# Performance work log

Hardware: AMD Instinct MI355X
Metric: run time of the kernel (lower is better)

Reference implementation:

```python
import jax, jax.numpy as jnp
import numpy as np

N_NODES = 100000
N_EDGES = 1600000
F_IN = 128
N_GRAPHS = 1000
NUM_CLASSES = 2


def setup_inputs() -> dict:
    key = jax.random.key(0)
    ks = jax.random.split(key, 12)
    x = jax.random.normal(ks[0], (N_NODES, F_IN), jnp.float32)
    edge_index = jax.random.randint(ks[1], (2, N_EDGES), 0, N_NODES, dtype=jnp.int32)
    edge_weight = jnp.ones((N_EDGES,), jnp.float32)
    node_graph_index = jnp.sort(
        jax.random.randint(ks[2], (N_NODES,), 0, N_GRAPHS, dtype=jnp.int32))
    s = 0.05
    params = {
        'W0': jax.random.normal(ks[3], (F_IN, 64), jnp.float32) * s,
        'b0': jnp.zeros((64,), jnp.float32),
        'W1': jax.random.normal(ks[4], (64, 32), jnp.float32) * s,
        'b1': jnp.zeros((32,), jnp.float32),
        'Wm1': jax.random.normal(ks[5], (32, 128), jnp.float32) * s,
        'bm1': jnp.zeros((128,), jnp.float32),
        'Wm2': jax.random.normal(ks[6], (128, NUM_CLASSES), jnp.float32) * s,
        'bm2': jnp.zeros((NUM_CLASSES,), jnp.float32),
    }
    return dict(x=x, edge_index=edge_index, edge_weight=edge_weight,
                node_graph_index=node_graph_index, **params)


def _gcn_norm(edge_index, edge_weight, n_nodes):
    # renormalization trick: add self-loops, D^-1/2 (A+I) D^-1/2
    loop = jnp.arange(n_nodes, dtype=edge_index.dtype)
    src = jnp.concatenate([edge_index[0], loop])
    dst = jnp.concatenate([edge_index[1], loop])
    w = jnp.concatenate([edge_weight, jnp.ones((n_nodes,), edge_weight.dtype)])
    deg = jax.ops.segment_sum(w, dst, num_segments=n_nodes)
    dinv = jnp.where(deg > 0, jax.lax.rsqrt(jnp.maximum(deg, 1e-12)), 0.0)
    norm_w = dinv[src] * w * dinv[dst]
    return src, dst, norm_w


def _gcn_layer(h, src, dst, norm_w, W, b, n_nodes):
    m = h @ W                                # [N, out] dense transform first
    msg = m[src] * norm_w[:, None]           # [E+N, out] irregular gather
    agg = jax.ops.segment_sum(msg, dst, num_segments=n_nodes)
    return jax.nn.relu(agg + b)


def reference(x, edge_index, edge_weight, node_graph_index,
              W0, b0, W1, b1, Wm1, bm1, Wm2, bm2):
    n_nodes = x.shape[0]
    src, dst, norm_w = _gcn_norm(edge_index, edge_weight, n_nodes)
    h = _gcn_layer(x, src, dst, norm_w, W0, b0, n_nodes)   # GCN 64 + relu
    # dropout is identity at inference (training=False default)
    h = _gcn_layer(h, src, dst, norm_w, W1, b1, n_nodes)   # GCN 32 + relu
    g = jax.ops.segment_sum(h, node_graph_index, num_segments=N_GRAPHS)  # sum_pool
    g = jax.nn.relu(g @ Wm1 + bm1)
    logits = g @ Wm2 + bm2
    return logits
```

## Files before the change

kernel.cpp:

```cpp
#include <hip/hip_runtime.h>
#include <hip/hip_bf16.h>

#define F_IN 128
#define NPB 256
#define NPB_SH 8
#define MAXB 512
#define CHUNK 4096
#define CAP 5120

typedef __attribute__((ext_vector_type(8))) short short8;
typedef __attribute__((ext_vector_type(4))) float f32x4;


__device__ __forceinline__ float bf2f(unsigned short u) {
    return __uint_as_float(((unsigned int)u) << 16);
}
__device__ __forceinline__ unsigned short f2bf(float f) {
    unsigned int x = __float_as_uint(f);
    x += 0x7FFFu + ((x >> 16) & 1u);
    return (unsigned short)(x >> 16);
}
__device__ __forceinline__ void bf8_fma(float w, uint4 r, float* a) {
    a[0] = fmaf(w, __uint_as_float(r.x << 16), a[0]);
    a[1] = fmaf(w, __uint_as_float(r.x & 0xFFFF0000u), a[1]);
    a[2] = fmaf(w, __uint_as_float(r.y << 16), a[2]);
    a[3] = fmaf(w, __uint_as_float(r.y & 0xFFFF0000u), a[3]);
    a[4] = fmaf(w, __uint_as_float(r.z << 16), a[4]);
    a[5] = fmaf(w, __uint_as_float(r.z & 0xFFFF0000u), a[5]);
    a[6] = fmaf(w, __uint_as_float(r.w << 16), a[6]);
    a[7] = fmaf(w, __uint_as_float(r.w & 0xFFFF0000u), a[7]);
}

__global__ __launch_bounds__(256) void prep_w_kernel(
    const float* __restrict__ W0, const float* __restrict__ W1,
    unsigned short* __restrict__ W0t, unsigned short* __restrict__ W1t,
    int* __restrict__ gcursor, float* __restrict__ Gbuf,
    int nbucket, int gtot) {
    int t = blockIdx.x * 256 + threadIdx.x;
    int stride = gridDim.x * 256;
    for (int o = t; o < 64 * 128; o += stride) {
        int n = o >> 7, k = o & 127;
        W0t[o] = f2bf(W0[k * 64 + n]);
    }
    for (int o = t; o < 32 * 64; o += stride) {
        int n = o >> 6, k = o & 63;
        W1t[o] = f2bf(W1[k * 32 + n]);
    }
    for (int o = t; o < nbucket; o += stride) gcursor[o] = 0;
    for (int o = t; o < gtot; o += stride) Gbuf[o] = 0.f;
}

__global__ __launch_bounds__(1024) void bucket_fused_kernel(
    const int* __restrict__ src, const int* __restrict__ dst,
    const float* __restrict__ ew, int* __restrict__ gcursor,
    int2* __restrict__ tmp, int E, int nbucket) {
    __shared__ int hist[MAXB];
    __shared__ int gbase[MAXB];
    const int tid = threadIdx.x;
    const int e0 = blockIdx.x * CHUNK;
    const int e1 = min(e0 + CHUNK, E);
    for (int b = tid; b < nbucket; b += 1024) hist[b] = 0;
    __syncthreads();
    const int e = e0 + (tid << 2);
    const bool vec = (e + 4 <= e1);
    const int nsc = vec ? 0 : max(0, e1 - e);
    int4 d4 = make_int4(0, 0, 0, 0);
    if (vec) {
        d4 = *(const int4*)(dst + e);
        atomicAdd(&hist[d4.x >> NPB_SH], 1);
        atomicAdd(&hist[d4.y >> NPB_SH], 1);
        atomicAdd(&hist[d4.z >> NPB_SH], 1);
        atomicAdd(&hist[d4.w >> NPB_SH], 1);
    } else {
        for (int j = 0; j < nsc; ++j) {
            int d = dst[e + j];
            ((int*)&d4)[j] = d;
            atomicAdd(&hist[d >> NPB_SH], 1);
        }
    }
    __syncthreads();
    for (int b = tid; b < nbucket; b += 1024) {
        int h = hist[b];
        gbase[b] = (h > 0) ? atomicAdd(&gcursor[b], h) : 0;
        hist[b] = 0;
    }
    __syncthreads();
    if (vec) {
        int4 s4 = *(const int4*)(src + e);
        float4 w4 = *(const float4*)(ew + e);
        {
            int d = d4.x, b = d >> NPB_SH;
            int r = atomicAdd(&hist[b], 1);
            tmp[(size_t)b * CAP + gbase[b] + r] =
                make_int2(s4.x | ((d & (NPB - 1)) << 17), __float_as_int(w4.x));
        }
        {
            int d = d4.y, b = d >> NPB_SH;
            int r = atomicAdd(&hist[b], 1);
            tmp[(size_t)b * CAP + gbase[b] + r] =
                make_int2(s4.y | ((d & (NPB - 1)) << 17), __float_as_int(w4.y));
        }
        {
            int d = d4.z, b = d >> NPB_SH;
            int r = atomicAdd(&hist[b], 1);
            tmp[(size_t)b * CAP + gbase[b] + r] =
                make_int2(s4.z | ((d & (NPB - 1)) << 17), __float_as_int(w4.z));
        }
        {
            int d = d4.w, b = d >> NPB_SH;
            int r = atomicAdd(&hist[b], 1);
            tmp[(size_t)b * CAP + gbase[b] + r] =
                make_int2(s4.w | ((d & (NPB - 1)) << 17), __float_as_int(w4.w));
        }
    } else {
        for (int j = 0; j < nsc; ++j) {
            int d = ((int*)&d4)[j];
            int b = d >> NPB_SH;
            int r = atomicAdd(&hist[b], 1);
            tmp[(size_t)b * CAP + gbase[b] + r] =
                make_int2(src[e + j] | ((d & (NPB - 1)) << 17), __float_as_int(ew[e + j]));
        }
    }
}

__global__ __launch_bounds__(1024) void csr_kernel(
    const int2* __restrict__ tmp, const int* __restrict__ gcursor,
    int2* __restrict__ es, int* __restrict__ rstart, int* __restrict__ rend,
    float* __restrict__ dinv, int N) {
    __shared__ int cnt[256];
    __shared__ float dw[256];
    __shared__ int off[256];
    __shared__ int cur[256];
    const int t = threadIdx.x;
    const int n0 = blockIdx.x << NPB_SH;
    const size_t seg = (size_t)blockIdx.x * CAP;
    if (t < 256) {
        cnt[t] = 0;
        dw[t] = 0.f;
    }
    __syncthreads();
    const int count = gcursor[blockIdx.x];
    const int pairs = count >> 1;
    for (int i = t; i < pairs; i += 1024) {
        int4 v = *(const int4*)(tmp + seg + 2 * i);
        int d0 = v.x >> 17, d1 = v.z >> 17;
        atomicAdd(&cnt[d0], 1);
        atomicAdd(&dw[d0], __int_as_float(v.y));
        atomicAdd(&cnt[d1], 1);
        atomicAdd(&dw[d1], __int_as_float(v.w));
    }
    if ((count & 1) && t == 0) {
        int2 e2 = tmp[seg + count - 1];
        int d = e2.x >> 17;
        atomicAdd(&cnt[d], 1);
        atomicAdd(&dw[d], __int_as_float(e2.y));
    }
    __syncthreads();
    if (t < 256) off[t] = cnt[t];
    __syncthreads();
    for (int o = 1; o < 256; o <<= 1) {
        int x = 0;
        if (t >= o && t < 256) x = off[t - o];
        __syncthreads();
        if (t < 256) off[t] += x;
        __syncthreads();
    }
    if (t < 256) {
        int v = cnt[t];
        int excl = off[t] - v;
        cur[t] = excl;
        int n = n0 + t;
        if (n < N) {
            rstart[n] = (int)seg + excl;
            rend[n] = (int)seg + excl + v;
            dinv[n] = rsqrtf(fmaxf(1.f + dw[t], 1e-12f));
        }
    }
    __syncthreads();
    for (int i = t; i < pairs; i += 1024) {
        int4 v = *(const int4*)(tmp + seg + 2 * i);
        int d0 = v.x >> 17, d1 = v.z >> 17;
        int r0 = atomicAdd(&cur[d0], 1);
        es[seg + r0] = make_int2(v.x & 0x1FFFF, v.y);
        int r1 = atomicAdd(&cur[d1], 1);
        es[seg + r1] = make_int2(v.z & 0x1FFFF, v.w);
    }
    if ((count & 1) && t == 0) {
        int2 e2 = tmp[seg + count - 1];
        int d = e2.x >> 17;
        int r = atomicAdd(&cur[d], 1);
        es[seg + r] = make_int2(e2.x & 0x1FFFF, e2.y);
    }
}

__global__ __launch_bounds__(256) void gemm1_mfma_kernel(
    const float* __restrict__ X, const unsigned short* __restrict__ W0t,
    const float* __restrict__ dinv, unsigned short* __restrict__ M, int N) {
    __shared__ unsigned short Bs[64][136];
    const int tid = threadIdx.x;
    for (int i = tid; i < 64 * 32; i += 256) {
        int n = i >> 5, k4 = i & 31;
        ushort4 v = ((const ushort4*)W0t)[i];
        *(ushort4*)&Bs[n][k4 * 4] = v;
    }
    __syncthreads();
    const int wave = tid >> 6, lane = tid & 63;
    const int m = lane & 15, q = lane >> 4;
    const int rowA = blockIdx.x * 64 + wave * 16 + m;
    const bool rok = rowA < N;
    const float* xrow = X + (size_t)rowA * 128;
    f32x4 acc[4] = {};
#pragma unroll
    for (int ks = 0; ks < 4; ++ks) {
        int k0 = ks * 32 + q * 8;
        float4 u0 = make_float4(0.f, 0.f, 0.f, 0.f);
        float4 u1 = make_float4(0.f, 0.f, 0.f, 0.f);
        if (rok) {
            u0 = *(const float4*)(xrow + k0);
            u1 = *(const float4*)(xrow + k0 + 4);
        }
        short8 a;
        a[0] = (short)f2bf(u0.x); a[1] = (short)f2bf(u0.y);
        a[2] = (short)f2bf(u0.z); a[3] = (short)f2bf(u0.w);
        a[4] = (short)f2bf(u1.x); a[5] = (short)f2bf(u1.y);
        a[6] = (short)f2bf(u1.z); a[7] = (short)f2bf(u1.w);
#pragma unroll
        for (int ct = 0; ct < 4; ++ct) {
            short8 b = *(const short8*)&Bs[ct * 16 + m][k0];
            acc[ct] = __builtin_amdgcn_mfma_f32_16x16x32_bf16(a, b, acc[ct], 0, 0, 0);
        }
    }
#pragma unroll
    for (int r = 0; r < 4; ++r) {
        int crow = blockIdx.x * 64 + wave * 16 + q * 4 + r;
        if (crow < N) {
            float d = dinv[crow];
#pragma unroll
            for (int ct = 0; ct < 4; ++ct)
                M[(size_t)crow * 64 + ct * 16 + m] = f2bf(acc[ct][r] * d);
        }
    }
}

__global__ __launch_bounds__(256) void gemm2_mfma_kernel(
    const unsigned short* __restrict__ H1, const unsigned short* __restrict__ W1t,
    const float* __restrict__ dinv, unsigned short* __restrict__ M, int N) {
    __shared__ unsigned short Bs[32][72];
    const int tid = threadIdx.x;
    for (int i = tid; i < 32 * 16; i += 256) {
        int n = i >> 4, k4 = i & 15;
        ushort4 v = ((const ushort4*)W1t)[i];
        *(ushort4*)&Bs[n][k4 * 4] = v;
    }
    __syncthreads();
    const int wave = tid >> 6, lane = tid & 63;
    const int m = lane & 15, q = lane >> 4;
    const int rowA = blockIdx.x * 64 + wave * 16 + m;
    const bool rok = rowA < N;
    const short8 az = {0, 0, 0, 0, 0, 0, 0, 0};
    f32x4 acc[2] = {};
#pragma unroll
    for (int ks = 0; ks < 2; ++ks) {
        int k0 = ks * 32 + q * 8;
        short8 a = rok ? *(const short8*)(H1 + (size_t)rowA * 64 + k0) : az;
#pragma unroll
        for (int ct = 0; ct < 2; ++ct) {
            short8 b = *(const short8*)&Bs[ct * 16 + m][k0];
            acc[ct] = __builtin_amdgcn_mfma_f32_16x16x32_bf16(a, b, acc[ct], 0, 0, 0);
        }
    }
#pragma unroll
    for (int r = 0; r < 4; ++r) {
        int crow = blockIdx.x * 64 + wave * 16 + q * 4 + r;
        if (crow < N) {
            float d = dinv[crow];
#pragma unroll
            for (int ct = 0; ct < 2; ++ct)
                M[(size_t)crow * 32 + ct * 16 + m] = f2bf(acc[ct][r] * d);
        }
    }
}

__global__ __launch_bounds__(256) void pull1_kernel(
    const int* __restrict__ rstart, const int* __restrict__ rend,
    const int2* __restrict__ es, const unsigned short* __restrict__ M,
    const float* __restrict__ dinv, const float* __restrict__ bias,
    unsigned short* __restrict__ H1, int N) {
    const int lane = threadIdx.x & 63;
    const int wave = threadIdx.x >> 6;
    const int nd = lane >> 5;
    const int node = blockIdx.x * 8 + wave * 2 + nd;
    if (node >= N) return;
    const int c = lane & 7;
    const int q = (lane >> 3) & 3;
    float acc[8] = {0.f, 0.f, 0.f, 0.f, 0.f, 0.f, 0.f, 0.f};
    if (q == 0) {
        uint4 r = *(const uint4*)(M + (size_t)node * 64 + c * 8);
        bf8_fma(1.f, r, acc);
    }
    const int b = rstart[node], e = rend[node];
    const int len = e - b;
    const int base = len >> 2, rem = len & 3;
    int p = b + q * base + min(q, rem);
    const int pe = p + base + (q < rem ? 1 : 0);
    for (; p + 2 <= pe; p += 2) {
        int4 v = *(const int4*)(es + p);
        uint4 r0 = *(const uint4*)(M + (size_t)v.x * 64 + c * 8);
        uint4 r1 = *(const uint4*)(M + (size_t)v.z * 64 + c * 8);
        bf8_fma(__int_as_float(v.y), r0, acc);
        bf8_fma(__int_as_float(v.w), r1, acc);
    }
    if (p < pe) {
        int2 ed = es[p];
        uint4 r = *(const uint4*)(M + (size_t)ed.x * 64 + c * 8);
        bf8_fma(__int_as_float(ed.y), r, acc);
    }
#pragma unroll
    for (int off = 8; off <= 16; off <<= 1)
#pragma unroll
        for (int k = 0; k < 8; ++k) acc[k] += __shfl_xor(acc[k], off);
    if (q == 0) {
        float d = dinv[node];
        const float* bp = bias + c * 8;
        float4 b0v = *(const float4*)(bp);
        float4 b1v = *(const float4*)(bp + 4);
        unsigned short o[8];
        o[0] = f2bf(fmaxf(fmaf(d, acc[0], b0v.x), 0.f));
        o[1] = f2bf(fmaxf(fmaf(d, acc[1], b0v.y), 0.f));
        o[2] = f2bf(fmaxf(fmaf(d, acc[2], b0v.z), 0.f));
        o[3] = f2bf(fmaxf(fmaf(d, acc[3], b0v.w), 0.f));
        o[4] = f2bf(fmaxf(fmaf(d, acc[4], b1v.x), 0.f));
        o[5] = f2bf(fmaxf(fmaf(d, acc[5], b1v.y), 0.f));
        o[6] = f2bf(fmaxf(fmaf(d, acc[6], b1v.z), 0.f));
        o[7] = f2bf(fmaxf(fmaf(d, acc[7], b1v.w), 0.f));
        uint4 pk;
        pk.x = (unsigned int)o[0] | ((unsigned int)o[1] << 16);
        pk.y = (unsigned int)o[2] | ((unsigned int)o[3] << 16);
        pk.z = (unsigned int)o[4] | ((unsigned int)o[5] << 16);
        pk.w = (unsigned int)o[6] | ((unsigned int)o[7] << 16);
        *(uint4*)(H1 + (size_t)node * 64 + c * 8) = pk;
    }
}

__global__ __launch_bounds__(256) void pull2_pool_kernel(
    const int* __restrict__ rstart, const int* __restrict__ rend,
    const int2* __restrict__ es, const unsigned short* __restrict__ M,
    const float* __restrict__ dinv, const float* __restrict__ bias,
    const int* __restrict__ ngi, float* __restrict__ g, int N) {
    __shared__ float4 sh[16][8];
    __shared__ int sgx[16];
    const int t = threadIdx.x;
    const int lane = t & 63;
    const int nl = t >> 4;
    const int node = blockIdx.x * 16 + nl;
    const int c = lane & 3;
    const int q = (lane >> 2) & 3;
    const bool valid = node < N;
    float acc[8] = {0.f, 0.f, 0.f, 0.f, 0.f, 0.f, 0.f, 0.f};
    if (valid) {
        if (q == 0) {
            uint4 r = *(const uint4*)(M + (size_t)node * 32 + c * 8);
            bf8_fma(1.f, r, acc);
        }
        const int b = rstart[node], e = rend[node];
        const int len = e - b;
        const int base = len >> 2, rem = len & 3;
        int p = b + q * base + min(q, rem);
        const int pe = p + base + (q < rem ? 1 : 0);
        for (; p + 2 <= pe; p += 2) {
            int4 v = *(const int4*)(es + p);
            uint4 r0 = *(const uint4*)(M + (size_t)v.x * 32 + c * 8);
            uint4 r1 = *(const uint4*)(M + (size_t)v.z * 32 + c * 8);
            bf8_fma(__int_as_float(v.y), r0, acc);
            bf8_fma(__int_as_float(v.w), r1, acc);
        }
        if (p < pe) {
            int2 ed = es[p];
            uint4 r = *(const uint4*)(M + (size_t)ed.x * 32 + c * 8);
            bf8_fma(__int_as_float(ed.y), r, acc);
        }
#pragma unroll
        for (int off = 4; off <= 8; off <<= 1)
#pragma unroll
            for (int k = 0; k < 8; ++k) acc[k] += __shfl_xor(acc[k], off);
    }
    if (q == 0) {
        float4 o0 = make_float4(0.f, 0.f, 0.f, 0.f);
        float4 o1 = make_float4(0.f, 0.f, 0.f, 0.f);
        if (valid) {
            float d = dinv[node];
            const float* bp = bias + c * 8;
            float4 b0v = *(const float4*)(bp);
            float4 b1v = *(const float4*)(bp + 4);
            o0.x = fmaxf(fmaf(d, acc[0], b0v.x), 0.f);
            o0.y = fmaxf(fmaf(d, acc[1], b0v.y), 0.f);
            o0.z = fmaxf(fmaf(d, acc[2], b0v.z), 0.f);
            o0.w = fmaxf(fmaf(d, acc[3], b0v.w), 0.f);
            o1.x = fmaxf(fmaf(d, acc[4], b1v.x), 0.f);
            o1.y = fmaxf(fmaf(d, acc[5], b1v.y), 0.f);
            o1.z = fmaxf(fmaf(d, acc[6], b1v.z), 0.f);
            o1.w = fmaxf(fmaf(d, acc[7], b1v.w), 0.f);
        }
        sh[nl][c * 2] = o0;
        sh[nl][c * 2 + 1] = o1;
        if (c == 0) sgx[nl] = valid ? ngi[node] : -1;
    }
    __syncthreads();
    if (t < 8) {
        int cc = t;
        float4 a = make_float4(0.f, 0.f, 0.f, 0.f);
        int cg = -1;
        for (int i = 0; i < 16; ++i) {
            int gi = sgx[i];
            if (gi < 0) continue;
            if (gi != cg) {
                if (cg >= 0) {
                    float* gp = g + cg * 32 + cc * 4;
                    atomicAdd(gp + 0, a.x); atomicAdd(gp + 1, a.y);
                    atomicAdd(gp + 2, a.z); atomicAdd(gp + 3, a.w);
                }
                cg = gi;
                a = sh[i][cc];
            } else {
                float4 tv = sh[i][cc];
                a.x += tv.x; a.y += tv.y; a.z += tv.z; a.w += tv.w;
            }
        }
        if (cg >= 0) {
            float* gp = g + cg * 32 + cc * 4;
            atomicAdd(gp + 0, a.x); atomicAdd(gp + 1, a.y);
            atomicAdd(gp + 2, a.z); atomicAdd(gp + 3, a.w);
        }
    }
}

__global__ __launch_bounds__(128) void mlp_kernel(
    const float* __restrict__ g, const float* __restrict__ Wm1,
    const float* __restrict__ bm1, const float* __restrict__ Wm2,
    const float* __restrict__ bm2, float* __restrict__ out) {
    __shared__ float sg[32];
    __shared__ float red[4];
    int b = blockIdx.x, t = threadIdx.x;
    if (t < 32) sg[t] = g[b * 32 + t];
    __syncthreads();
    float acc = bm1[t];
#pragma unroll
    for (int k = 0; k < 32; ++k) acc = fmaf(sg[k], Wm1[k * 128 + t], acc);
    float h = fmaxf(acc, 0.f);
    float p0 = h * Wm2[t * 2 + 0];
    float p1 = h * Wm2[t * 2 + 1];
#pragma unroll
    for (int off = 32; off >= 1; off >>= 1) {
        p0 += __shfl_xor(p0, off);
        p1 += __shfl_xor(p1, off);
    }
    if ((t & 63) == 0) {
        red[(t >> 6) * 2 + 0] = p0;
        red[(t >> 6) * 2 + 1] = p1;
    }
    __syncthreads();
    if (t < 2) out[b * 2 + t] = bm2[t] + red[t] + red[2 + t];
}


extern "C" void kernel_launch(void* const* d_in, const int* in_sizes, int n_in,
                              void* d_out, int out_size, void* d_ws, size_t ws_size,
                              hipStream_t stream) {
    const float* x   = (const float*)d_in[0];
    const int*   ei  = (const int*)d_in[1];
    const float* ew  = (const float*)d_in[2];
    const int*   ngi = (const int*)d_in[3];
    const float* W0  = (const float*)d_in[4];
    const float* b0  = (const float*)d_in[5];
    const float* W1  = (const float*)d_in[6];
    const float* b1  = (const float*)d_in[7];
    const float* Wm1 = (const float*)d_in[8];
    const float* bm1 = (const float*)d_in[9];
    const float* Wm2 = (const float*)d_in[10];
    const float* bm2 = (const float*)d_in[11];
    float* out = (float*)d_out;

    const int N = in_sizes[0] / F_IN;
    const int E = in_sizes[1] / 2;
    const int G = out_size / 2;
    const int* srcp = ei;
    const int* dstp = ei + E;
    const int NBUCKET = (N + NPB - 1) >> NPB_SH;
    const int NBLK = (E + CHUNK - 1) / CHUNK;

    char* wsb = (char*)d_ws;
    size_t off = 0;
    auto alloc = [&](size_t bytes) {
        char* p = wsb + off;
        off += (bytes + 255) & ~(size_t)255;
        return p;
    };
    float* dinv     = (float*)alloc((size_t)N * 4);
    int*   gcursor  = (int*)  alloc((size_t)NBUCKET * 4);
    int*   rstart   = (int*)  alloc((size_t)N * 4);
    int*   rend     = (int*)  alloc((size_t)N * 4);
    int2*  tmp      = (int2*) alloc((size_t)NBUCKET * CAP * 8);
    int2*  es       = (int2*) alloc((size_t)NBUCKET * CAP * 8);
    unsigned short* W0t = (unsigned short*)alloc(64 * 128 * 2);
    unsigned short* W1t = (unsigned short*)alloc(32 * 64 * 2);
    unsigned short* M   = (unsigned short*)alloc((size_t)N * 64 * 2);
    unsigned short* H1  = (unsigned short*)alloc((size_t)N * 64 * 2);
    float* Gbuf     = (float*)alloc((size_t)G * 32 * 4);
    unsigned short* m1p = M;

    prep_w_kernel<<<8, 256, 0, stream>>>(W0, W1, W0t, W1t, gcursor, Gbuf, NBUCKET, G * 32);
    bucket_fused_kernel<<<NBLK, 1024, 0, stream>>>(srcp, dstp, ew, gcursor, tmp, E, NBUCKET);
    csr_kernel<<<NBUCKET, 1024, 0, stream>>>(tmp, gcursor, es, rstart, rend, dinv, N);

    gemm1_mfma_kernel<<<(N + 63) / 64, 256, 0, stream>>>(x, W0t, dinv, M, N);
    pull1_kernel<<<(N + 7) / 8, 256, 0, stream>>>(rstart, rend, es, M, dinv, b0, H1, N);

    gemm2_mfma_kernel<<<(N + 63) / 64, 256, 0, stream>>>(H1, W1t, dinv, m1p, N);
    pull2_pool_kernel<<<(N + 15) / 16, 256, 0, stream>>>(rstart, rend, es, m1p, dinv, b1, ngi, Gbuf, N);

    mlp_kernel<<<G, 128, 0, stream>>>(Gbuf, Wm1, bm1, Wm2, bm2, out);
}
```

Before: 240.2 us.

## Replace bucketed two-pass CSR build with fixed-capacity per-node edge slots

The two-kernel bucket-then-sort CSR construction is replaced by a single kernel. It scatters each edge into a fixed 64-slot region per destination node using global atomic counters, and accumulates degree weights with unsafe float atomics. The dinv computation moves into the first GEMM epilogue, the pull kernels read the per-node counts directly, and the pooling atomics switch to unsafeAtomicAdd. This removes one kernel launch and the intermediate tmp pass, in exchange for scattered global atomics and a larger, sparse edge buffer. It also silently overflows into the next node's slots if any node has more than 64 in-edges.

After: 351.1 us. +46.2%, slower.

```diff
diff --git a/kernel.cpp b/kernel.cpp
--- a/kernel.cpp
+++ b/kernel.cpp
@@ -2,11 +2,7 @@
 #include <hip/hip_bf16.h>
 
 #define F_IN 128
-#define NPB 256
-#define NPB_SH 8
-#define MAXB 512
-#define CHUNK 4096
-#define CAP 5120
+#define CAPN 64
 
 typedef __attribute__((ext_vector_type(8))) short short8;
 typedef __attribute__((ext_vector_type(4))) float f32x4;
@@ -30,12 +26,15 @@
     a[6] = fmaf(w, __uint_as_float(r.w << 16), a[6]);
     a[7] = fmaf(w, __uint_as_float(r.w & 0xFFFF0000u), a[7]);
 }
+__device__ __forceinline__ void fadd_global(float* p, float v) {
+    unsafeAtomicAdd(p, v);
+}
 
 __global__ __launch_bounds__(256) void prep_w_kernel(
     const float* __restrict__ W0, const float* __restrict__ W1,
     unsigned short* __restrict__ W0t, unsigned short* __restrict__ W1t,
-    int* __restrict__ gcursor, float* __restrict__ Gbuf,
-    int nbucket, int gtot) {
+    int* __restrict__ ncnt, float* __restrict__ dw,
+    float* __restrict__ Gbuf, int N, int gtot) {
     int t = blockIdx.x * 256 + threadIdx.x;
     int stride = gridDim.x * 256;
     for (int o = t; o < 64 * 128; o += stride) {
@@ -46,156 +45,56 @@
         int n = o >> 6, k = o & 63;
         W1t[o] = f2bf(W1[k * 32 + n]);
     }
-    for (int o = t; o < nbucket; o += stride) gcursor[o] = 0;
+    for (int o = t; o < N; o += stride) {
+        ncnt[o] = 0;
+        dw[o] = 0.f;
+    }
     for (int o = t; o < gtot; o += stride) Gbuf[o] = 0.f;
 }
 
-__global__ __launch_bounds__(1024) void bucket_fused_kernel(
+__global__ __launch_bounds__(256) void build_csr_kernel(
     const int* __restrict__ src, const int* __restrict__ dst,
-    const float* __restrict__ ew, int* __restrict__ gcursor,
-    int2* __restrict__ tmp, int E, int nbucket) {
-    __shared__ int hist[MAXB];
-    __shared__ int gbase[MAXB];
-    const int tid = threadIdx.x;
-    const int e0 = blockIdx.x * CHUNK;
-    const int e1 = min(e0 + CHUNK, E);
-    for (int b = tid; b < nbucket; b += 1024) hist[b] = 0;
-    __syncthreads();
-    const int e = e0 + (tid << 2);
-    const bool vec = (e + 4 <= e1);
-    const int nsc = vec ? 0 : max(0, e1 - e);
-    int4 d4 = make_int4(0, 0, 0, 0);
-    if (vec) {
-        d4 = *(const int4*)(dst + e);
-        atomicAdd(&hist[d4.x >> NPB_SH], 1);
-        atomicAdd(&hist[d4.y >> NPB_SH], 1);
-        atomicAdd(&hist[d4.z >> NPB_SH], 1);
-        atomicAdd(&hist[d4.w >> NPB_SH], 1);
-    } else {
-        for (int j = 0; j < nsc; ++j) {
-            int d = dst[e + j];
-            ((int*)&d4)[j] = d;
-            atomicAdd(&hist[d >> NPB_SH], 1);
-        }
-    }
-    __syncthreads();
-    for (int b = tid; b < nbucket; b += 1024) {
-        int h = hist[b];
-        gbase[b] = (h > 0) ? atomicAdd(&gcursor[b], h) : 0;
-        hist[b] = 0;
-    }
-    __syncthreads();
-    if (vec) {
+    const float* __restrict__ ew, int* __restrict__ ncnt,
+    float* __restrict__ dw, int2* __restrict__ es, int E) {
+    const int e = (blockIdx.x * 256 + threadIdx.x) << 2;
+    if (e + 4 <= E) {
+        int4 d4 = *(const int4*)(dst + e);
         int4 s4 = *(const int4*)(src + e);
         float4 w4 = *(const float4*)(ew + e);
         {
-            int d = d4.x, b = d >> NPB_SH;
-            int r = atomicAdd(&hist[b], 1);
-            tmp[(size_t)b * CAP + gbase[b] + r] =
-                make_int2(s4.x | ((d & (NPB - 1)) << 17), __float_as_int(w4.x));
+            int r = atomicAdd(&ncnt[d4.x], 1);
+            es[(size_t)d4.x * CAPN + r] = make_int2(s4.x, __float_as_int(w4.x));
+            fadd_global(&dw[d4.x], w4.x);
         }
         {
-            int d = d4.y, b = d >> NPB_SH;
-            int r = atomicAdd(&hist[b], 1);
-            tmp[(size_t)b * CAP + gbase[b] + r] =
-                make_int2(s4.y | ((d & (NPB - 1)) << 17), __float_as_int(w4.y));
+            int r = atomicAdd(&ncnt[d4.y], 1);
+            es[(size_t)d4.y * CAPN + r] = make_int2(s4.y, __float_as_int(w4.y));
+            fadd_global(&dw[d4.y], w4.y);
         }
         {
-            int d = d4.z, b = d >> NPB_SH;
-            int r = atomicAdd(&hist[b], 1);
-            tmp[(size_t)b * CAP + gbase[b] + r] =
-                make_int2(s4.z | ((d & (NPB - 1)) << 17), __float_as_int(w4.z));
+            int r = atomicAdd(&ncnt[d4.z], 1);
+            es[(size_t)d4.z * CAPN + r] = make_int2(s4.z, __float_as_int(w4.z));
+            fadd_global(&dw[d4.z], w4.z);
         }
         {
-            int d = d4.w, b = d >> NPB_SH;
-            int r = atomicAdd(&hist[b], 1);
-            tmp[(size_t)b * CAP + gbase[b] + r] =
-                make_int2(s4.w | ((d & (NPB - 1)) << 17), __float_as_int(w4.w));
+            int r = atomicAdd(&ncnt[d4.w], 1);
+            es[(size_t)d4.w * CAPN + r] = make_int2(s4.w, __float_as_int(w4.w));
+            fadd_global(&dw[d4.w], w4.w);
         }
     } else {
-        for (int j = 0; j < nsc; ++j) {
-            int d = ((int*)&d4)[j];
-            int b = d >> NPB_SH;
-            int r = atomicAdd(&hist[b], 1);
-            tmp[(size_t)b * CAP + gbase[b] + r] =
-                make_int2(src[e + j] | ((d & (NPB - 1)) << 17), __float_as_int(ew[e + j]));
-        }
-    }
-}
-
-__global__ __launch_bounds__(1024) void csr_kernel(
-    const int2* __restrict__ tmp, const int* __restrict__ gcursor,
-    int2* __restrict__ es, int* __restrict__ rstart, int* __restrict__ rend,
-    float* __restrict__ dinv, int N) {
-    __shared__ int cnt[256];
-    __shared__ float dw[256];
-    __shared__ int off[256];
-    __shared__ int cur[256];
-    const int t = threadIdx.x;
-    const int n0 = blockIdx.x << NPB_SH;
-    const size_t seg = (size_t)blockIdx.x * CAP;
-    if (t < 256) {
-        cnt[t] = 0;
-        dw[t] = 0.f;
-    }
-    __syncthreads();
-    const int count = gcursor[blockIdx.x];
-    const int pairs = count >> 1;
-    for (int i = t; i < pairs; i += 1024) {
-        int4 v = *(const int4*)(tmp + seg + 2 * i);
-        int d0 = v.x >> 17, d1 = v.z >> 17;
-        atomicAdd(&cnt[d0], 1);
-        atomicAdd(&dw[d0], __int_as_float(v.y));
-        atomicAdd(&cnt[d1], 1);
-        atomicAdd(&dw[d1], __int_as_float(v.w));
-    }
-    if ((count & 1) && t == 0) {
-        int2 e2 = tmp[seg + count - 1];
-        int d = e2.x >> 17;
-        atomicAdd(&cnt[d], 1);
-        atomicAdd(&dw[d], __int_as_float(e2.y));
-    }
-    __syncthreads();
-    if (t < 256) off[t] = cnt[t];
-    __syncthreads();
-    for (int o = 1; o < 256; o <<= 1) {
-        int x = 0;
-        if (t >= o && t < 256) x = off[t - o];
-        __syncthreads();
-        if (t < 256) off[t] += x;
-        __syncthreads();
-    }
-    if (t < 256) {
-        int v = cnt[t];
-        int excl = off[t] - v;
-        cur[t] = excl;
-        int n = n0 + t;
-        if (n < N) {
-            rstart[n] = (int)seg + excl;
-            rend[n] = (int)seg + excl + v;
-            dinv[n] = rsqrtf(fmaxf(1.f + dw[t], 1e-12f));
-        }
-    }
-    __syncthreads();
-    for (int i = t; i < pairs; i += 1024) {
-        int4 v = *(const int4*)(tmp + seg + 2 * i);
-        int d0 = v.x >> 17, d1 = v.z >> 17;
-        int r0 = atomicAdd(&cur[d0], 1);
-        es[seg + r0] = make_int2(v.x & 0x1FFFF, v.y);
-        int r1 = atomicAdd(&cur[d1], 1);
-        es[seg + r1] = make_int2(v.z & 0x1FFFF, v.w);
-    }
-    if ((count & 1) && t == 0) {
-        int2 e2 = tmp[seg + count - 1];
-        int d = e2.x >> 17;
-        int r = atomicAdd(&cur[d], 1);
-        es[seg + r] = make_int2(e2.x & 0x1FFFF, e2.y);
+        for (int j = e; j < E; ++j) {
+            int d = dst[j];
+            int r = atomicAdd(&ncnt[d], 1);
+            es[(size_t)d * CAPN + r] = make_int2(src[j], __float_as_int(ew[j]));
+            fadd_global(&dw[d], ew[j]);
+        }
     }
 }
 
 __global__ __launch_bounds__(256) void gemm1_mfma_kernel(
     const float* __restrict__ X, const unsigned short* __restrict__ W0t,
-    const float* __restrict__ dinv, unsigned short* __restrict__ M, int N) {
+    const float* __restrict__ dw, float* __restrict__ dinv,
+    unsigned short* __restrict__ M, int N) {
     __shared__ unsigned short Bs[64][136];
     const int tid = threadIdx.x;
     for (int i = tid; i < 64 * 32; i += 256) {
@@ -234,10 +133,11 @@
     for (int r = 0; r < 4; ++r) {
         int crow = blockIdx.x * 64 + wave * 16 + q * 4 + r;
         if (crow < N) {
-            float d = dinv[crow];
+            float dv = rsqrtf(fmaxf(1.f + dw[crow], 1e-12f));
+            if (m == 0) dinv[crow] = dv;
 #pragma unroll
             for (int ct = 0; ct < 4; ++ct)
-                M[(size_t)crow * 64 + ct * 16 + m] = f2bf(acc[ct][r] * d);
+                M[(size_t)crow * 64 + ct * 16 + m] = f2bf(acc[ct][r] * dv);
         }
     }
 }
@@ -282,10 +182,9 @@
 }
 
 __global__ __launch_bounds__(256) void pull1_kernel(
-    const int* __restrict__ rstart, const int* __restrict__ rend,
-    const int2* __restrict__ es, const unsigned short* __restrict__ M,
-    const float* __restrict__ dinv, const float* __restrict__ bias,
-    unsigned short* __restrict__ H1, int N) {
+    const int* __restrict__ ncnt, const int2* __restrict__ es,
+    const unsigned short* __restrict__ M, const float* __restrict__ dinv,
+    const float* __restrict__ bias, unsigned short* __restrict__ H1, int N) {
     const int lane = threadIdx.x & 63;
     const int wave = threadIdx.x >> 6;
     const int nd = lane >> 5;
@@ -298,8 +197,8 @@
         uint4 r = *(const uint4*)(M + (size_t)node * 64 + c * 8);
         bf8_fma(1.f, r, acc);
     }
-    const int b = rstart[node], e = rend[node];
-    const int len = e - b;
+    const int b = node * CAPN;
+    const int len = ncnt[node];
     const int base = len >> 2, rem = len & 3;
     int p = b + q * base + min(q, rem);
     const int pe = p + base + (q < rem ? 1 : 0);
@@ -343,10 +242,10 @@
 }
 
 __global__ __launch_bounds__(256) void pull2_pool_kernel(
-    const int* __restrict__ rstart, const int* __restrict__ rend,
-    const int2* __restrict__ es, const unsigned short* __restrict__ M,
-    const float* __restrict__ dinv, const float* __restrict__ bias,
-    const int* __restrict__ ngi, float* __restrict__ g, int N) {
+    const int* __restrict__ ncnt, const int2* __restrict__ es,
+    const unsigned short* __restrict__ M, const float* __restrict__ dinv,
+    const float* __restrict__ bias, const int* __restrict__ ngi,
+    float* __restrict__ g, int N) {
     __shared__ float4 sh[16][8];
     __shared__ int sgx[16];
     const int t = threadIdx.x;
@@ -362,8 +261,8 @@
             uint4 r = *(const uint4*)(M + (size_t)node * 32 + c * 8);
             bf8_fma(1.f, r, acc);
         }
-        const int b = rstart[node], e = rend[node];
-        const int len = e - b;
+        const int b = node * CAPN;
+        const int len = ncnt[node];
         const int base = len >> 2, rem = len & 3;
         int p = b + q * base + min(q, rem);
         const int pe = p + base + (q < rem ? 1 : 0);
@@ -416,8 +315,8 @@
             if (gi != cg) {
                 if (cg >= 0) {
                     float* gp = g + cg * 32 + cc * 4;
-                    atomicAdd(gp + 0, a.x); atomicAdd(gp + 1, a.y);
-                    atomicAdd(gp + 2, a.z); atomicAdd(gp + 3, a.w);
+                    fadd_global(gp + 0, a.x); fadd_global(gp + 1, a.y);
+                    fadd_global(gp + 2, a.z); fadd_global(gp + 3, a.w);
                 }
                 cg = gi;
                 a = sh[i][cc];
@@ -428,8 +327,8 @@
         }
         if (cg >= 0) {
             float* gp = g + cg * 32 + cc * 4;
-            atomicAdd(gp + 0, a.x); atomicAdd(gp + 1, a.y);
-            atomicAdd(gp + 2, a.z); atomicAdd(gp + 3, a.w);
+            fadd_global(gp + 0, a.x); fadd_global(gp + 1, a.y);
+            fadd_global(gp + 2, a.z); fadd_global(gp + 3, a.w);
         }
     }
 }
@@ -485,8 +384,6 @@
     const int G = out_size / 2;
     const int* srcp = ei;
     const int* dstp = ei + E;
-    const int NBUCKET = (N + NPB - 1) >> NPB_SH;
-    const int NBLK = (E + CHUNK - 1) / CHUNK;
 
     char* wsb = (char*)d_ws;
     size_t off = 0;
@@ -496,11 +393,9 @@
         return p;
     };
     float* dinv     = (float*)alloc((size_t)N * 4);
-    int*   gcursor  = (int*)  alloc((size_t)NBUCKET * 4);
-    int*   rstart   = (int*)  alloc((size_t)N * 4);
-    int*   rend     = (int*)  alloc((size_t)N * 4);
-    int2*  tmp      = (int2*) alloc((size_t)NBUCKET * CAP * 8);
-    int2*  es       = (int2*) alloc((size_t)NBUCKET * CAP * 8);
+    float* dw       = (float*)alloc((size_t)N * 4);
+    int*   ncnt     = (int*)  alloc((size_t)N * 4);
+    int2*  es       = (int2*) alloc((size_t)N * CAPN * 8);
     unsigned short* W0t = (unsigned short*)alloc(64 * 128 * 2);
     unsigned short* W1t = (unsigned short*)alloc(32 * 64 * 2);
     unsigned short* M   = (unsigned short*)alloc((size_t)N * 64 * 2);
@@ -508,15 +403,14 @@
     float* Gbuf     = (float*)alloc((size_t)G * 32 * 4);
     unsigned short* m1p = M;
 
-    prep_w_kernel<<<8, 256, 0, stream>>>(W0, W1, W0t, W1t, gcursor, Gbuf, NBUCKET, G * 32);
-    bucket_fused_kernel<<<NBLK, 1024, 0, stream>>>(srcp, dstp, ew, gcursor, tmp, E, NBUCKET);
-    csr_kernel<<<NBUCKET, 1024, 0, stream>>>(tmp, gcursor, es, rstart, rend, dinv, N);
-
-    gemm1_mfma_kernel<<<(N + 63) / 64, 256, 0, stream>>>(x, W0t, dinv, M, N);
-    pull1_kernel<<<(N + 7) / 8, 256, 0, stream>>>(rstart, rend, es, M, dinv, b0, H1, N);
+    prep_w_kernel<<<64, 256, 0, stream>>>(W0, W1, W0t, W1t, ncnt, dw, Gbuf, N, G * 32);
+    build_csr_kernel<<<(E + 1023) / 1024, 256, 0, stream>>>(srcp, dstp, ew, ncnt, dw, es, E);
+
+    gemm1_mfma_kernel<<<(N + 63) / 64, 256, 0, stream>>>(x, W0t, dw, dinv, M, N);
+    pull1_kernel<<<(N + 7) / 8, 256, 0, stream>>>(ncnt, es, M, dinv, b0, H1, N);
 
     gemm2_mfma_kernel<<<(N + 63) / 64, 256, 0, stream>>>(H1, W1t, dinv, m1p, N);
-    pull2_pool_kernel<<<(N + 15) / 16, 256, 0, stream>>>(rstart, rend, es, m1p, dinv, b1, ngi, Gbuf, N);
+    pull2_pool_kernel<<<(N + 15) / 16, 256, 0, stream>>>(ncnt, es, m1p, dinv, b1, ngi, Gbuf, N);
 
     mlp_kernel<<<G, 128, 0, stream>>>(Gbuf, Wm1, bm1, Wm2, bm2, out);
 }
```
